# Kernel optimization log

Measured on AMD Instinct MI355X. Metric: run time of the kernel, lower is better.

Reference implementation:

```python
import math
import jax, jax.numpy as jnp
import numpy as np

B, S, HIDDEN = 1, 8192, 2048
NUM_HEADS = 16
HEAD_DIM = HIDDEN // NUM_HEADS
NUM_FW = 4
FW_DIM = HIDDEN // NUM_FW
D_H = FW_DIM  # inter_multi = 1.0
WINDOW = 256
CHUNK = 2048
ROPE_THETA = 500000.0
BASE_LR_INV = float(np.log(np.expm1(0.001)))  # inv_softplus(1e-3)


def rms_norm(x, w, eps=1e-6):
    return x * jax.lax.rsqrt(jnp.mean(x * x, axis=-1, keepdims=True) + eps) * w


def apply_rope(q, k, theta):
    D = q.shape[-1]
    inv = 1.0 / (theta ** (jnp.arange(0, D, 2, dtype=jnp.float32) / D))
    t = jnp.arange(q.shape[1], dtype=jnp.float32)
    f = t[:, None] * inv[None, :]  # [S, D/2]
    cos = jnp.cos(f)[None, :, None, :]
    sin = jnp.sin(f)[None, :, None, :]
    def ap(x):
        x1, x2 = jnp.split(x, 2, axis=-1)
        return jnp.concatenate([x1 * cos - x2 * sin, x2 * cos + x1 * sin], axis=-1)
    return ap(q), ap(k)


def sliding_window_attn(q, k, v, window):
    # q,k,v: [B,S,H,D]; causal window of `window` tokens incl. self (flash (window-1, 0))
    B_, S_, H_, D_ = q.shape
    W = window
    nc = S_ // W
    def blk(x):
        return x.transpose(0, 2, 1, 3).reshape(B_, H_, nc, W, D_)
    qb, kb, vb = blk(q), blk(k), blk(v)
    pad = jnp.zeros((B_, H_, 1, W, D_), q.dtype)
    k2 = jnp.concatenate([jnp.concatenate([pad, kb[:, :, :-1]], 2), kb], 3)  # [B,H,nc,2W,D]
    v2 = jnp.concatenate([jnp.concatenate([pad, vb[:, :, :-1]], 2), vb], 3)
    r = jnp.arange(W)[:, None]
    j = jnp.arange(2 * W)[None, :]
    base = (j >= r + 1) & (j <= W + r)  # causal + within-window
    keypos = (jnp.arange(nc)[:, None, None] - 1) * W + j[None]
    mask = base[None] & (keypos >= 0)  # [nc,W,2W]
    scores = jnp.einsum('bhnqd,bhnkd->bhnqk', qb, k2) * (1.0 / math.sqrt(D_))
    scores = jnp.where(mask[None, None], scores, -jnp.inf)
    p = jax.nn.softmax(scores, axis=-1)
    o = jnp.einsum('bhnqk,bhnkd->bhnqd', p, v2)
    return o.reshape(B_, H_, S_, D_).transpose(0, 2, 1, 3)


def ttt_swiglu(fq, fk, fv, l0, l1, l2, w0, w1, w2, chunk):
    # fq/fk/fv: [BN,S,d]; l*: [BN,S,1]; w0,w2: [BN,dh,d]; w1: [BN,d,dh]
    BN, S_, d = fq.shape
    nc = S_ // chunk
    def ch(x):
        return x.reshape(BN, nc, chunk, x.shape[-1]).transpose(1, 0, 2, 3)
    xs = (ch(fq), ch(fk), ch(fv), ch(l0), ch(l1), ch(l2))
    def step(carry, x):
        w0c, w1c, w2c = carry
        qi, ki, vi, lr0, lr1, lr2 = x
        # apply current fast weights to chunk queries (SwiGLU MLP)
        o = jnp.einsum('bch,boh->bco',
                       jax.nn.silu(jnp.einsum('bcd,bhd->bch', qi, w0c)) * jnp.einsum('bcd,bhd->bch', qi, w2c),
                       w1c)
        # manual gradient of dot-product TTT loss L = -sum(v * f(k))
        g = jnp.einsum('bcd,bhd->bch', ki, w0c)
        hm = jnp.einsum('bcd,bhd->bch', ki, w2c)
        sg = jax.nn.sigmoid(g)
        silu_g = g * sg
        hid = silu_g * hm
        dhid = jnp.einsum('bco,boh->bch', vi, w1c)
        dhm = dhid * silu_g
        dg = dhid * hm
        dgp = dg * (sg * (1.0 + g * (1.0 - sg)))  # silu backprop
        w0n = w0c + jnp.einsum('bch,bcd->bhd', dgp * lr0, ki)
        w2n = w2c + jnp.einsum('bch,bcd->bhd', dhm * lr2, ki)
        w1n = w1c + jnp.einsum('bco,bch->boh', vi * lr1, hid)
        return (w0n, w1n, w2n), o
    _, outs = jax.lax.scan(step, (w0, w1, w2), xs)
    return outs.transpose(1, 0, 2, 3).reshape(BN, S_, d)


def setup_inputs():
    key = jax.random.key(0)
    ks = jax.random.split(key, 8)
    h = HIDDEN
    return {
        'hidden_states': jax.random.normal(ks[0], (B, S, h), jnp.float32),
        'qkv_w': jax.random.normal(ks[1], (3 * h, h), jnp.float32) * 0.02,
        'q_norm_w': jnp.ones((h,), jnp.float32),
        'k_norm_w': jnp.ones((h,), jnp.float32),
        'qk_scale': jnp.ones((h, 2), jnp.float32),
        'qk_offset': jnp.zeros((h, 2), jnp.float32),
        'lr_w': jax.random.normal(ks[2], (3 * NUM_FW, h), jnp.float32) * 0.02,
        'lr_b': jnp.zeros((3 * NUM_FW,), jnp.float32),
        'w0': jax.random.normal(ks[3], (NUM_FW, D_H, FW_DIM), jnp.float32) / math.sqrt(FW_DIM),
        'w1': jax.random.normal(ks[4], (NUM_FW, FW_DIM, D_H), jnp.float32) / math.sqrt(D_H),
        'w2': jax.random.normal(ks[5], (NUM_FW, D_H, FW_DIM), jnp.float32) / math.sqrt(FW_DIM),
        'ttt_norm_w': jnp.ones((FW_DIM,), jnp.float32),
        'o_proj_w': jax.random.normal(ks[6], (h, h), jnp.float32) * 0.02,
    }


def reference(hidden_states, qkv_w, q_norm_w, k_norm_w, qk_scale, qk_offset,
              lr_w, lr_b, w0, w1, w2, ttt_norm_w, o_proj_w):
    qkv = hidden_states @ qkv_w.T
    q, k, v = jnp.split(qkv, 3, axis=-1)
    q = rms_norm(q, q_norm_w)
    k = rms_norm(k, k_norm_w)
    # rescale q/k for the fast-weight path
    fq = q * qk_scale[:, 0] + qk_offset[:, 0]
    fk = k * qk_scale[:, 1] + qk_offset[:, 1]
    fv = v
    # windowed RoPE attention path
    qh = q.reshape(B, S, NUM_HEADS, HEAD_DIM)
    kh = k.reshape(B, S, NUM_HEADS, HEAD_DIM)
    vh = v.reshape(B, S, NUM_HEADS, HEAD_DIM)
    qh, kh = apply_rope(qh, kh, ROPE_THETA)
    attn_o = sliding_window_attn(qh, kh, vh, WINDOW).reshape(B, S, HIDDEN)
    # fast-weight (TTT) path: silu + per-head l2-norm on q/k
    fq = jax.nn.silu(fq).reshape(B, S, NUM_FW, FW_DIM)
    fk = jax.nn.silu(fk).reshape(B, S, NUM_FW, FW_DIM)
    fv = jax.nn.silu(fv).reshape(B, S, NUM_FW, FW_DIM)
    fq = fq / jnp.maximum(jnp.linalg.norm(fq, axis=-1, keepdims=True), 1e-12)
    fk = fk / jnp.maximum(jnp.linalg.norm(fk, axis=-1, keepdims=True), 1e-12)
    def flat(x):
        return x.transpose(0, 2, 1, 3).reshape(B * NUM_FW, S, FW_DIM)
    # per-token learning rates (mamba parameterization)
    lr = jax.nn.softplus(hidden_states @ lr_w.T + lr_b + BASE_LR_INV)  # [B,S,3*NH]
    l0, l1, l2 = jnp.split(lr, 3, axis=-1)
    def flat_lr(x):
        return x.transpose(0, 2, 1).reshape(B * NUM_FW, S, 1)
    def bcast(w):
        return jnp.broadcast_to(w[None], (B,) + w.shape).reshape(B * NUM_FW, w.shape[1], w.shape[2])
    o_fast = ttt_swiglu(flat(fq), flat(fk), flat(fv),
                        flat_lr(l0), flat_lr(l1), flat_lr(l2),
                        bcast(w0), bcast(w1), bcast(w2), CHUNK)
    o_fast = rms_norm(o_fast.reshape(B, NUM_FW, S, FW_DIM), ttt_norm_w)
    o_fast = o_fast.transpose(0, 2, 1, 3).reshape(B, S, HIDDEN)
    return (attn_o + o_fast) @ o_proj_w.T
```

## Files before the change

### kernel.cpp

```cpp
#include <hip/hip_runtime.h>
#include <hip/hip_bf16.h>

typedef __hip_bfloat16 bf16;
typedef __bf16 bft;
typedef bft bf16x8 __attribute__((ext_vector_type(8)));
typedef bft bf16x4 __attribute__((ext_vector_type(4)));
typedef float f32x4 __attribute__((ext_vector_type(4)));

#define S_LEN 8192
#define HID   2048
#define QKV3  6144
#define NH    16
#define HD    128
#define NFW   4
#define FD    512
#define CHUNK_LEN 2048
#define NCHUNK 4
#define BASE_LR_INV (-6.9072552f)
#define QKP 136
#define VSP 72
#define PSP 76

__device__ __forceinline__ float bf2f(bf16 x){ return __bfloat162float(x); }
__device__ __forceinline__ bf16  f2bf(float x){ return __float2bfloat16(x); }
__device__ __forceinline__ float sigm(float x){ return 1.f/(1.f+__expf(-x)); }
__device__ __forceinline__ float siluf(float x){ return x/(1.f+__expf(-x)); }
__device__ __forceinline__ float wave_sum(float v){
  #pragma unroll
  for(int off=32; off; off>>=1) v += __shfl_xor(v, off, 64);
  return v;
}

template<int N>
__device__ __forceinline__ void waitcnt_vm(){
  static_assert(N==0||N==2||N==4||N==8, "unsupported vmcnt");
  if constexpr (N==0)      asm volatile("s_waitcnt vmcnt(0)" ::: "memory");
  else if constexpr (N==2) asm volatile("s_waitcnt vmcnt(2)" ::: "memory");
  else if constexpr (N==4) asm volatile("s_waitcnt vmcnt(4)" ::: "memory");
  else                     asm volatile("s_waitcnt vmcnt(8)" ::: "memory");
}

template<int ROWS>
__device__ __forceinline__ void stage(const bft* __restrict__ src, long ld,
                                      bft* dst, int tid)
{
  const int lane = tid & 63, wv = tid >> 6;
  #pragma unroll
  for (int i = 0; i < ROWS/64; ++i) {
    const int r0 = wv*16 + i*64;
    const int row = r0 + (lane >> 2);
    const int g = (lane & 3) ^ ((row >> 1) & 3);
    const bft* gp = src + (size_t)row*ld + g*8;
    bft* lp = dst + (size_t)r0*32;
    __builtin_amdgcn_global_load_lds(
        (const __attribute__((address_space(1))) void*)gp,
        (__attribute__((address_space(3))) void*)lp, 16, 0, 0);
  }
}

template<int BM,int BN,int EPI>
__global__ __launch_bounds__(256) void mgemm_k(
    const bft* __restrict__ A, const bft* __restrict__ B, void* __restrict__ Cv,
    bft* __restrict__ Cd, bft* __restrict__ Ct, int K,
    long lda, long ldb, long ldc, long sA, long sB, long sC)
{
  constexpr int AM = BM/32, AN = BN/32;
  constexpr int LPS = BM/64 + BN/64;
  __shared__ __align__(16) bft As[4][BM*32];
  __shared__ __align__(16) bft Bs[4][BN*32];
  const int tid = threadIdx.x;
  const int z = blockIdx.z;
  A += (size_t)z * sA;
  B += (size_t)z * sB;
  const size_t m0 = (size_t)blockIdx.y * BM, n0 = (size_t)blockIdx.x * BN;
  const int wv = tid >> 6, lane = tid & 63;
  const int wm = (wv & 1) * (BM/2), wn = (wv >> 1) * (BN/2);
  const int fr = lane & 15;
  const int fsw = ((lane >> 4) ^ ((fr >> 1) & 3)) * 8;

  f32x4 acc[AM][AN];
  #pragma unroll
  for (int i=0;i<AM;i++)
    #pragma unroll
    for (int j=0;j<AN;j++) acc[i][j] = (f32x4){0.f,0.f,0.f,0.f};

  const bft* Ab = A + m0*lda;
  const bft* Bb = B + n0*ldb;
  const int NS = K >> 5;

  stage<BM>(Ab,      lda, As[0], tid);
  stage<BN>(Bb,      ldb, Bs[0], tid);
  stage<BM>(Ab + 32, lda, As[1], tid);
  stage<BN>(Bb + 32, ldb, Bs[1], tid);

  auto compute = [&](int s){
    const bft* Ap = As[s & 3];
    const bft* Bp = Bs[s & 3];
    bf16x8 af[AM], bfv[AN];
    #pragma unroll
    for (int mi=0; mi<AM; mi++)
      af[mi] = *(const bf16x8*)(Ap + (size_t)(wm + mi*16 + fr)*32 + fsw);
    #pragma unroll
    for (int ni=0; ni<AN; ni++)
      bfv[ni] = *(const bf16x8*)(Bp + (size_t)(wn + ni*16 + fr)*32 + fsw);
    __builtin_amdgcn_s_setprio(1);
    #pragma unroll
    for (int mi=0; mi<AM; mi++)
      #pragma unroll
      for (int ni=0; ni<AN; ni++)
        acc[mi][ni] = __builtin_amdgcn_mfma_f32_16x16x32_bf16(af[mi], bfv[ni], acc[mi][ni], 0, 0, 0);
    __builtin_amdgcn_s_setprio(0);
  };

  for (int s = 0; s < NS - 2; ++s) {
    const int kt = (s + 2) * 32;
    stage<BM>(Ab + kt, lda, As[(s+2)&3], tid);
    stage<BN>(Bb + kt, ldb, Bs[(s+2)&3], tid);
    waitcnt_vm<2*LPS>();
    __builtin_amdgcn_s_barrier();
    asm volatile("" ::: "memory");
    compute(s);
  }
  waitcnt_vm<LPS>();
  __builtin_amdgcn_s_barrier();
  asm volatile("" ::: "memory");
  compute(NS - 2);
  waitcnt_vm<0>();
  __builtin_amdgcn_s_barrier();
  asm volatile("" ::: "memory");
  compute(NS - 1);

  const int er = (lane >> 4) * 4;
  const int ec = lane & 15;
  #pragma unroll
  for (int mi=0; mi<AM; mi++){
    #pragma unroll
    for (int ni=0; ni<AN; ni++){
      #pragma unroll
      for (int r=0; r<4; r++){
        size_t row = m0 + wm + mi*16 + er + r;
        size_t col = n0 + wn + ni*16 + ec;
        size_t idx = (size_t)z*sC + row*ldc + col;
        float v = acc[mi][ni][r];
        if constexpr (EPI == 0){
          ((bft*)Cv)[idx] = (bft)v;
        } else if constexpr (EPI == 1){
          ((float*)Cv)[idx] = v;
        } else {
          float nv = ((float*)Cv)[idx] + v;
          ((float*)Cv)[idx] = nv;
          Cd[idx] = (bft)nv;
          if (Ct) Ct[(size_t)z*FD*FD + col*FD + row] = (bft)nv;
        }
      }
    }
  }
}

template<int BM,int BN,int EPI>
static inline void mgemm(hipStream_t st, const bft* A, const bft* B, void* C,
    bft* Cd, bft* Ct, int M, int N, int K, long lda, long ldb, long ldc,
    int batch, long sA, long sB, long sC)
{
  dim3 g(N/BN, M/BM, batch);
  mgemm_k<BM,BN,EPI><<<g, 256, 0, st>>>(A, B, C, Cd, Ct, K, lda, ldb, ldc, sA, sB, sC);
}

__device__ __forceinline__ void stage8(const bft* __restrict__ src, long ld,
                                       bft* dst, int tid)
{
  const int lane = tid & 63, wv = tid >> 6;
  #pragma unroll
  for (int i = 0; i < 2; ++i) {
    const int r0 = wv*16 + i*128;
    const int row = r0 + (lane >> 2);
    const int g = (lane & 3) ^ ((row >> 1) & 3);
    const bft* gp = src + (size_t)row*ld + g*8;
    bft* lp = dst + (size_t)r0*32;
    __builtin_amdgcn_global_load_lds(
        (const __attribute__((address_space(1))) void*)gp,
        (__attribute__((address_space(3))) void*)lp, 16, 0, 0);
  }
}

template<int EPI>
__global__ __launch_bounds__(512, 2) void mgemm8_k(
    const bft* __restrict__ A, const bft* __restrict__ B, void* __restrict__ Cv,
    int K, long lda, long ldb, long ldc)
{
  __shared__ __align__(16) bft As[4][256*32];
  __shared__ __align__(16) bft Bs[4][256*32];
  const int tid = threadIdx.x;

  const int gx = (int)gridDim.x;
  const int nwg = (int)(gridDim.x * gridDim.y);
  int lin = (int)(blockIdx.y * gridDim.x + blockIdx.x);
  if ((nwg & 7) == 0) lin = (lin & 7) * (nwg >> 3) + (lin >> 3);
  const size_t m0 = (size_t)(lin / gx) * 256;
  const size_t n0 = (size_t)(lin % gx) * 256;

  const int wv = tid >> 6, lane = tid & 63;
  const int wm = (wv & 1) * 128, wn = (wv >> 1) * 64;
  const int fr = lane & 15;
  const int fsw = ((lane >> 4) ^ ((fr >> 1) & 3)) * 8;

  f32x4 acc[8][4];
  #pragma unroll
  for (int i=0;i<8;i++)
    #pragma unroll
    for (int j=0;j<4;j++) acc[i][j] = (f32x4){0.f,0.f,0.f,0.f};

  const bft* Ab = A + m0*lda;
  const bft* Bb = B + n0*ldb;
  const int NS = K >> 5;

  stage8(Ab,      lda, As[0], tid);
  stage8(Bb,      ldb, Bs[0], tid);
  stage8(Ab + 32, lda, As[1], tid);
  stage8(Bb + 32, ldb, Bs[1], tid);

  auto compute = [&](int s){
    const bft* Ap = As[s & 3];
    const bft* Bp = Bs[s & 3];
    bf16x8 af[8], bv[4];
    #pragma unroll
    for (int mi=0; mi<8; mi++)
      af[mi] = *(const bf16x8*)(Ap + (size_t)(wm + mi*16 + fr)*32 + fsw);
    #pragma unroll
    for (int ni=0; ni<4; ni++)
      bv[ni] = *(const bf16x8*)(Bp + (size_t)(wn + ni*16 + fr)*32 + fsw);
    __builtin_amdgcn_s_setprio(1);
    #pragma unroll
    for (int mi=0; mi<8; mi++)
      #pragma unroll
      for (int ni=0; ni<4; ni++)
        acc[mi][ni] = __builtin_amdgcn_mfma_f32_16x16x32_bf16(af[mi], bv[ni], acc[mi][ni], 0, 0, 0);
    __builtin_amdgcn_s_setprio(0);
  };

  for (int s = 0; s < NS - 2; ++s) {
    const int kt = (s + 2) * 32;
    stage8(Ab + kt, lda, As[(s+2)&3], tid);
    stage8(Bb + kt, ldb, Bs[(s+2)&3], tid);
    asm volatile("s_waitcnt vmcnt(8)" ::: "memory");
    __builtin_amdgcn_s_barrier();
    asm volatile("" ::: "memory");
    compute(s);
  }
  asm volatile("s_waitcnt vmcnt(4)" ::: "memory");
  __builtin_amdgcn_s_barrier();
  asm volatile("" ::: "memory");
  compute(NS - 2);
  asm volatile("s_waitcnt vmcnt(0)" ::: "memory");
  __builtin_amdgcn_s_barrier();
  asm volatile("" ::: "memory");
  compute(NS - 1);

  const int er = (lane >> 4) * 4;
  const int ec = lane & 15;
  #pragma unroll
  for (int mi=0; mi<8; mi++){
    #pragma unroll
    for (int ni=0; ni<4; ni++){
      #pragma unroll
      for (int r=0; r<4; r++){
        size_t row = m0 + wm + mi*16 + er + r;
        size_t col = n0 + wn + ni*16 + ec;
        size_t idx = row*ldc + col;
        float v = acc[mi][ni][r];
        if constexpr (EPI == 0) ((bft*)Cv)[idx] = (bft)v;
        else                    ((float*)Cv)[idx] = v;
      }
    }
  }
}

template<int EPI>
static inline void mgemm8(hipStream_t st, const bft* A, const bft* B, void* C,
                          int M, int N, int K, long lda, long ldb, long ldc)
{
  dim3 g(N/256, M/256, 1);
  mgemm8_k<EPI><<<g, 512, 0, st>>>(A, B, C, K, lda, ldb, ldc);
}

__global__ __launch_bounds__(256) void cvt_k(const float* __restrict__ s,
    bft* __restrict__ d)
{
  size_t i = ((size_t)blockIdx.x*256 + threadIdx.x) * 8;
  const float4 v0 = *(const float4*)(s + i);
  const float4 v1 = *(const float4*)(s + i + 4);
  bf16x8 b;
  b[0]=(bft)v0.x; b[1]=(bft)v0.y; b[2]=(bft)v0.z; b[3]=(bft)v0.w;
  b[4]=(bft)v1.x; b[5]=(bft)v1.y; b[6]=(bft)v1.z; b[7]=(bft)v1.w;
  *(bf16x8*)(d + i) = b;
}

__global__ __launch_bounds__(256) void tr_k(const bft* __restrict__ in,
    bft* __restrict__ out, long ldin, long sIn, long sOut)
{
  __shared__ __align__(16) bft t[64][72];
  const int c0 = blockIdx.x*64, r0 = blockIdx.y*64;
  in  += (size_t)blockIdx.z * sIn;
  out += (size_t)blockIdx.z * sOut;
  const int tid = threadIdx.x;
  #pragma unroll
  for (int i=0;i<2;i++){
    int e = tid + i*256;
    int r = e >> 3, c8 = (e & 7) * 8;
    *(bf16x8*)&t[r][c8] = *(const bf16x8*)(in + (size_t)(r0+r)*ldin + c0 + c8);
  }
  __syncthreads();
  #pragma unroll
  for (int i=0;i<2;i++){
    int e = tid + i*256;
    int c = e >> 3, r8 = (e & 7) * 8;
    bf16x8 v;
    #pragma unroll
    for (int j=0;j<8;j++) v[j] = t[r8+j][c];
    *(bf16x8*)(out + (size_t)(c0+c)*CHUNK_LEN + r0 + r8) = v;
  }
}

__global__ __launch_bounds__(256) void tcw1_k(const float* __restrict__ w1,
    bft* __restrict__ w1tb)
{
  size_t idx = (size_t)blockIdx.x*256 + threadIdx.x;
  int z = (int)(idx >> 18);
  int h = (int)((idx >> 9) & 511);
  int o = (int)(idx & 511);
  w1tb[idx] = (bft)w1[(size_t)z*FD*FD + (size_t)o*FD + h];
}

__global__ __launch_bounds__(256) void vt_k(const bf16* __restrict__ qkv,
    bft* __restrict__ vT)
{
  __shared__ __align__(16) bft t[64*QKP];
  const int s0 = blockIdx.x * 64;
  const int h  = blockIdx.y;
  const int tid = threadIdx.x;
  #pragma unroll
  for (int i=0;i<4;i++){
    int e = tid + i*256;
    int rr = e >> 4, doff = (e & 15) * 8;
    *(bf16x8*)(t + rr*QKP + doff) =
        *(const bf16x8*)((const bft*)qkv + (size_t)(s0+rr)*QKV3 + 2*HID + h*HD + doff);
  }
  __syncthreads();
  #pragma unroll
  for (int it=0; it<4; it++){
    int d = (tid >> 3) + it*32;
    int so8 = (tid & 7) * 8;
    bf16x8 v;
    #pragma unroll
    for (int j=0;j<8;j++) v[j] = t[(so8+j)*QKP + d];
    *(bf16x8*)(vT + ((size_t)(h*HD + d))*S_LEN + s0 + so8) = v;
  }
}

__global__ void rope_k(float* __restrict__ rc, float* __restrict__ rs){
  int pos = blockIdx.x, d = threadIdx.x;
  float inv = 1.f / powf(500000.0f, (float)d * (1.0f/64.0f));
  float ang = (float)pos * inv;
  rc[pos*64+d] = cosf(ang);
  rs[pos*64+d] = sinf(ang);
}

__global__ __launch_bounds__(256) void lr_k(const float* __restrict__ hidden,
    const float* __restrict__ lr_w, const float* __restrict__ lr_b,
    float* __restrict__ lro)
{
  __shared__ float hrow[HID];
  __shared__ float red[4][12];
  int s = blockIdx.x, tid = threadIdx.x;
  for(int i=0;i<HID/256;i++) hrow[tid+256*i] = hidden[(size_t)s*HID + tid + 256*i];
  __syncthreads();
  float part[12];
  #pragma unroll
  for(int o=0;o<12;o++) part[o]=0.f;
  for(int i=0;i<HID/256;i++){
    int j = tid + 256*i;
    float h = hrow[j];
    #pragma unroll
    for(int o=0;o<12;o++) part[o] += h * lr_w[o*HID + j];
  }
  int lane = tid & 63, w = tid >> 6;
  #pragma unroll
  for(int o=0;o<12;o++){
    float v = wave_sum(part[o]);
    if(lane==0) red[w][o] = v;
  }
  __syncthreads();
  if(tid < 12){
    float v = red[0][tid]+red[1][tid]+red[2][tid]+red[3][tid] + lr_b[tid] + BASE_LR_INV;
    float sp = (v > 20.f) ? v : log1pf(expf(v));
    lro[s*12 + tid] = sp;
  }
}

__global__ __launch_bounds__(256) void e2a_k(
    bf16* __restrict__ qkv,
    const float* __restrict__ qnw, const float* __restrict__ knw)
{
  __shared__ float red[8];
  int s = blockIdx.x, tid = threadIdx.x;
  int lane = tid & 63, w = tid >> 6;
  float qv[8], kv[8];
  float sq = 0.f, sk = 0.f;
  size_t base = (size_t)s*QKV3;
  #pragma unroll
  for(int i=0;i<8;i++){
    int j = tid*8 + i;
    qv[i] = bf2f(qkv[base + j]);
    kv[i] = bf2f(qkv[base + HID + j]);
    sq += qv[i]*qv[i]; sk += kv[i]*kv[i];
  }
  sq = wave_sum(sq); sk = wave_sum(sk);
  if(lane==0){ red[w] = sq; red[4+w] = sk; }
  __syncthreads();
  float rq = rsqrtf((red[0]+red[1]+red[2]+red[3])*(1.f/HID) + 1e-6f);
  float rk = rsqrtf((red[4]+red[5]+red[6]+red[7])*(1.f/HID) + 1e-6f);
  #pragma unroll
  for(int i=0;i<8;i++){
    int j = tid*8 + i;
    qkv[base + j]       = f2bf(qv[i]*rq*qnw[j]);
    qkv[base + HID + j] = f2bf(kv[i]*rk*knw[j]);
  }
}

__global__ __launch_bounds__(256) void e2b_k(
    bf16* __restrict__ qkv,
    const float* __restrict__ qks, const float* __restrict__ qko)
{
  int s = blockIdx.x, tid = threadIdx.x;
  size_t base = (size_t)s*QKV3;
  float a[8], b[8], vv[8];
  float ga = 0.f, gb2 = 0.f;
  #pragma unroll
  for(int i=0;i<8;i++){
    int j = tid*8 + i;
    float qn = bf2f(qkv[base + j]);
    float kn = bf2f(qkv[base + HID + j]);
    float v  = bf2f(qkv[base + 2*HID + j]);
    a[i] = siluf(qn*qks[2*j]   + qko[2*j]);
    b[i] = siluf(kn*qks[2*j+1] + qko[2*j+1]);
    vv[i] = siluf(v);
    ga += a[i]*a[i]; gb2 += b[i]*b[i];
  }
  ga = wave_sum(ga); gb2 = wave_sum(gb2);
  float iq = 1.f / fmaxf(sqrtf(ga), 1e-12f);
  float ik = 1.f / fmaxf(sqrtf(gb2), 1e-12f);
  #pragma unroll
  for(int i=0;i<8;i++){
    int j = tid*8 + i;
    qkv[base + j]         = f2bf(a[i]*iq);
    qkv[base + HID + j]   = f2bf(b[i]*ik);
    qkv[base + 2*HID + j] = f2bf(vv[i]);
  }
}

__global__ __launch_bounds__(256) void attn_k(
    const bf16* __restrict__ qkv, const bft* __restrict__ vT,
    const float* __restrict__ rc, const float* __restrict__ rs,
    float* __restrict__ attn)
{
  __shared__ __align__(16) bft Qs[64*QKP];
  __shared__ __align__(16) bft Ks[64*QKP];
  __shared__ __align__(16) bft Vs[128*VSP];
  __shared__ __align__(16) bft Ps[64*PSP];
  const int head = blockIdx.x >> 7;
  const int Q0 = (blockIdx.x & 127) * 64;
  const int tid = threadIdx.x;
  const int hb = head * HD;
  const int lane = tid & 63;
  const int wm = (tid >> 6) * 16;
  const int fr = lane & 15, fko = (lane >> 4) * 8;
  const int rbase = (lane >> 4) * 4;

  #pragma unroll
  for(int i=0;i<16;i++){
    int e = tid + i*256;
    int rr = e >> 6, d = e & 63;
    int qpos = Q0 + rr;
    size_t b = (size_t)qpos*QKV3 + hb;
    float x1 = bf2f(qkv[b + d]);
    float x2 = bf2f(qkv[b + d + 64]);
    float c = rc[qpos*64 + d], sn = rs[qpos*64 + d];
    Qs[rr*QKP + d]      = (bft)(x1*c - x2*sn);
    Qs[rr*QKP + d + 64] = (bft)(x2*c + x1*sn);
  }
  __syncthreads();
  bf16x8 qf[4];
  #pragma unroll
  for (int kk=0;kk<4;kk++)
    qf[kk] = *(const bf16x8*)(Qs + (wm+fr)*QKP + kk*32 + fko);

  f32x4 Ot[8];
  #pragma unroll
  for (int i=0;i<8;i++) Ot[i] = (f32x4){0.f,0.f,0.f,0.f};
  float m4[4], l4[4];
  #pragma unroll
  for (int r=0;r<4;r++){ m4[r] = -INFINITY; l4[r] = 0.f; }

  for (int kt=0; kt<5; kt++){
    const int kb = Q0 - 256 + kt*64;
    if (kb < 0) continue;
    __syncthreads();
    #pragma unroll
    for(int i=0;i<16;i++){
      int e = tid + i*256;
      int rr = e >> 6, d = e & 63;
      int kpos = kb + rr;
      size_t b = (size_t)kpos*QKV3 + HID + hb;
      float x1 = bf2f(qkv[b + d]);
      float x2 = bf2f(qkv[b + d + 64]);
      float c = rc[kpos*64 + d], sn = rs[kpos*64 + d];
      Ks[rr*QKP + d]      = (bft)(x1*c - x2*sn);
      Ks[rr*QKP + d + 64] = (bft)(x2*c + x1*sn);
    }
    {
      int d = tid >> 1, koff = (tid & 1) * 32;
      const bft* vrow = vT + ((size_t)(hb + d))*S_LEN + kb + koff;
      bft* lrow = Vs + d*VSP + koff;
      #pragma unroll
      for (int j8=0;j8<4;j8++)
        *(bf16x8*)(lrow + j8*8) = *(const bf16x8*)(vrow + j8*8);
    }
    __syncthreads();

    f32x4 st[4];
    #pragma unroll
    for (int nt=0;nt<4;nt++){
      f32x4 acc = (f32x4){0.f,0.f,0.f,0.f};
      #pragma unroll
      for (int kk=0;kk<4;kk++){
        bf16x8 kf = *(const bf16x8*)(Ks + (nt*16+fr)*QKP + kk*32 + fko);
        acc = __builtin_amdgcn_mfma_f32_16x16x32_bf16(qf[kk], kf, acc, 0, 0, 0);
      }
      st[nt] = acc;
    }

    float pv[4][4];
    #pragma unroll
    for (int r=0;r<4;r++){
      int qpos = Q0 + wm + rbase + r;
      float sm[4];
      float mx = -INFINITY;
      #pragma unroll
      for (int nt=0;nt<4;nt++){
        int kpos = kb + nt*16 + fr;
        bool valid = (kpos > qpos - 256) && (kpos <= qpos);
        float s = valid ? st[nt][r] * 0.088388347648318447f : -INFINITY;
        sm[nt] = s;
        mx = fmaxf(mx, s);
      }
      mx = fmaxf(mx, __shfl_xor(mx, 1, 64));
      mx = fmaxf(mx, __shfl_xor(mx, 2, 64));
      mx = fmaxf(mx, __shfl_xor(mx, 4, 64));
      mx = fmaxf(mx, __shfl_xor(mx, 8, 64));
      float mnew = fmaxf(m4[r], mx);
      float alpha = (mnew == -INFINITY) ? 1.f : __expf(m4[r] - mnew);
      float ps = 0.f;
      #pragma unroll
      for (int nt=0;nt<4;nt++){
        float p = (sm[nt] == -INFINITY) ? 0.f : __expf(sm[nt] - mnew);
        pv[nt][r] = p;
        ps += p;
      }
      ps += __shfl_xor(ps, 1, 64);
      ps += __shfl_xor(ps, 2, 64);
      ps += __shfl_xor(ps, 4, 64);
      ps += __shfl_xor(ps, 8, 64);
      l4[r] = l4[r]*alpha + ps;
      m4[r] = mnew;
      #pragma unroll
      for (int ct=0;ct<8;ct++) Ot[ct][r] *= alpha;
    }

    #pragma unroll
    for (int r=0;r<4;r++){
      int row = wm + rbase + r;
      #pragma unroll
      for (int nt=0;nt<4;nt++)
        Ps[row*PSP + nt*16 + fr] = (bft)pv[nt][r];
    }
    bf16x8 af[2];
    #pragma unroll
    for (int kk=0;kk<2;kk++){
      const bft* pp = Ps + (wm+fr)*PSP + kk*32 + fko;
      bf16x4 lo = *(const bf16x4*)pp;
      bf16x4 hi = *(const bf16x4*)(pp+4);
      bf16x8 a;
      #pragma unroll
      for (int j=0;j<4;j++){ a[j]=lo[j]; a[j+4]=hi[j]; }
      af[kk]=a;
    }
    #pragma unroll
    for (int ct=0;ct<8;ct++)
      #pragma unroll
      for (int kk=0;kk<2;kk++){
        bf16x8 bv = *(const bf16x8*)(Vs + (ct*16+fr)*VSP + kk*32 + fko);
        Ot[ct] = __builtin_amdgcn_mfma_f32_16x16x32_bf16(af[kk], bv, Ot[ct], 0, 0, 0);
      }
  }

  #pragma unroll
  for (int r=0;r<4;r++){
    float invl = 1.f / l4[r];
    int qpos = Q0 + wm + rbase + r;
    size_t ob = (size_t)qpos*HID + hb;
    #pragma unroll
    for (int ct=0;ct<8;ct++)
      attn[ob + ct*16 + fr] = Ot[ct][r] * invl;
  }
}

__global__ __launch_bounds__(256) void e3_k(
    const bf16* __restrict__ g, const bf16* __restrict__ hm,
    bf16* __restrict__ qg, const bf16* __restrict__ qm,
    bf16* __restrict__ hid)
{
  size_t idx = (size_t)blockIdx.x*256 + threadIdx.x;
  float opre = siluf(bf2f(qg[idx])) * bf2f(qm[idx]);
  hid[idx] = f2bf(siluf(bf2f(g[idx])) * bf2f(hm[idx]));
  qg[idx]  = f2bf(opre);
}

__global__ __launch_bounds__(256) void e4_k(
    bf16* __restrict__ g, bf16* __restrict__ hm, bf16* __restrict__ dhid,
    const bf16* __restrict__ qkv, const float* __restrict__ lrb, int cbase)
{
  size_t idx = (size_t)blockIdx.x*256 + threadIdx.x;
  int h  = (int)(idx >> 20);
  int ci = (int)((idx >> 9) & 2047);
  int d  = (int)(idx & 511);
  int s  = cbase + ci;
  float l0  = lrb[s*12 + h];
  float l1  = lrb[s*12 + 4 + h];
  float l2v = lrb[s*12 + 8 + h];
  float gg = bf2f(g[idx]), hv = bf2f(hm[idx]), dh = bf2f(dhid[idx]);
  float sg = sigm(gg);
  float silu_g = gg * sg;
  float dhm = dh * silu_g;
  float dg  = dh * hv;
  float dgp = dg * (sg * (1.f + gg * (1.f - sg)));
  float fvv = bf2f(qkv[(size_t)s*QKV3 + 2*HID + h*FD + d]);
  g[idx]    = f2bf(dgp * l0);
  hm[idx]   = f2bf(dhm * l2v);
  dhid[idx] = f2bf(fvv * l1);
}

__global__ __launch_bounds__(256) void e5_k(const float* __restrict__ attn,
    const bf16* __restrict__ ofc, const float* __restrict__ tnw,
    bf16* __restrict__ qkv, int cbase)
{
  int ci = blockIdx.x, tid = threadIdx.x;
  int s = cbase + ci;
  int lane = tid & 63, w = tid >> 6;
  float o[8]; float ss = 0.f;
  size_t ob = ((size_t)w*CHUNK_LEN + ci)*FD + (size_t)lane*8;
  #pragma unroll
  for(int i=0;i<8;i++){ o[i] = bf2f(ofc[ob+i]); ss += o[i]*o[i]; }
  ss = wave_sum(ss);
  float inv = rsqrtf(ss*(1.f/FD) + 1e-6f);
  size_t xb = (size_t)s*QKV3 + w*FD + (size_t)lane*8;
  size_t ab = (size_t)s*HID  + w*FD + (size_t)lane*8;
  #pragma unroll
  for(int i=0;i<8;i++){
    int d = lane*8 + i;
    qkv[xb+i] = f2bf(attn[ab+i] + o[i]*inv*tnw[d]);
  }
}

extern "C" void kernel_launch(void* const* d_in, const int* in_sizes, int n_in,
                              void* d_out, int out_size, void* d_ws, size_t ws_size,
                              hipStream_t stream)
{
  (void)in_sizes; (void)n_in; (void)out_size;
  const float* hidden   = (const float*)d_in[0];
  const float* qkv_w    = (const float*)d_in[1];
  const float* q_norm_w = (const float*)d_in[2];
  const float* k_norm_w = (const float*)d_in[3];
  const float* qk_scale = (const float*)d_in[4];
  const float* qk_off   = (const float*)d_in[5];
  const float* lr_w     = (const float*)d_in[6];
  const float* lr_b     = (const float*)d_in[7];
  const float* w0_in    = (const float*)d_in[8];
  const float* w1_in    = (const float*)d_in[9];
  const float* w2_in    = (const float*)d_in[10];
  const float* ttt_nw   = (const float*)d_in[11];
  const float* o_proj   = (const float*)d_in[12];
  float* out = (float*)d_out;

  char* p = (char*)d_ws;
  auto alloc = [&](size_t n){ char* r = p; p += (n + 255) & ~(size_t)255; return (void*)r; };

  bf16*  qkv   = (bf16*) alloc((size_t)S_LEN*QKV3*sizeof(bf16));
  float* lrb   = (float*)alloc((size_t)S_LEN*12*sizeof(float));
  float* rc    = (float*)alloc((size_t)S_LEN*64*sizeof(float));
  float* rs    = (float*)alloc((size_t)S_LEN*64*sizeof(float));
  float* w0s   = (float*)alloc((size_t)NFW*FD*FD*sizeof(float));
  float* w1s   = (float*)alloc((size_t)NFW*FD*FD*sizeof(float));
  float* w2s   = (float*)alloc((size_t)NFW*FD*FD*sizeof(float));
  bft*   w1tb  = (bft*)  alloc((size_t)NFW*FD*FD*sizeof(bft));
  bft*   w0b   = (bft*)  alloc((size_t)NFW*FD*FD*sizeof(bft));
  bft*   w1b   = (bft*)  alloc((size_t)NFW*FD*FD*sizeof(bft));
  bft*   w2b   = (bft*)  alloc((size_t)NFW*FD*FD*sizeof(bft));
  bf16*  gb    = (bf16*) alloc((size_t)NFW*CHUNK_LEN*FD*sizeof(bf16));
  bf16*  hmb   = (bf16*) alloc((size_t)NFW*CHUNK_LEN*FD*sizeof(bf16));
  bf16*  qgb   = (bf16*) alloc((size_t)NFW*CHUNK_LEN*FD*sizeof(bf16));
  bf16*  qmb   = (bf16*) alloc((size_t)NFW*CHUNK_LEN*FD*sizeof(bf16));
  bf16*  hidb  = (bf16*) alloc((size_t)NFW*CHUNK_LEN*FD*sizeof(bf16));
  bf16*  ofc   = (bf16*) alloc((size_t)NFW*CHUNK_LEN*FD*sizeof(bf16));
  bft*   fkT   = (bft*)  alloc((size_t)NFW*FD*CHUNK_LEN*sizeof(bft));
  bft*   hidT  = (bft*)  alloc((size_t)NFW*FD*CHUNK_LEN*sizeof(bft));
  bft*   a2T   = (bft*)  alloc((size_t)NFW*FD*CHUNK_LEN*sizeof(bft));
  bft*   a1T   = (bft*)  alloc((size_t)NFW*FD*CHUNK_LEN*sizeof(bft));

  if ((size_t)(p - (char*)d_ws) > ws_size) return;

  bft* hidden_bf = (bft*)gb;
  bft* qkvw_bf   = (bft*)fkT;
  bft* vT        = (bft*)fkT;
  bft* opw_bf    = (bft*)hidb;

  float* attn = out;

  hipMemcpyAsync(w0s, w0_in, (size_t)NFW*FD*FD*sizeof(float), hipMemcpyDeviceToDevice, stream);
  hipMemcpyAsync(w1s, w1_in, (size_t)NFW*FD*FD*sizeof(float), hipMemcpyDeviceToDevice, stream);
  hipMemcpyAsync(w2s, w2_in, (size_t)NFW*FD*FD*sizeof(float), hipMemcpyDeviceToDevice, stream);

  rope_k<<<S_LEN, 64, 0, stream>>>(rc, rs);
  lr_k<<<S_LEN, 256, 0, stream>>>(hidden, lr_w, lr_b, lrb);
  tcw1_k<<<NFW*FD*FD/256, 256, 0, stream>>>(w1_in, w1tb);
  cvt_k<<<(NFW*FD*FD)/2048, 256, 0, stream>>>(w0_in, w0b);
  cvt_k<<<(NFW*FD*FD)/2048, 256, 0, stream>>>(w1_in, w1b);
  cvt_k<<<(NFW*FD*FD)/2048, 256, 0, stream>>>(w2_in, w2b);
  cvt_k<<<(S_LEN*HID)/2048, 256, 0, stream>>>(hidden, hidden_bf);
  cvt_k<<<(QKV3*HID)/2048, 256, 0, stream>>>(qkv_w, qkvw_bf);

  mgemm8<0>(stream, hidden_bf, qkvw_bf, (void*)qkv, S_LEN, QKV3, HID, HID, HID, QKV3);

  e2a_k<<<S_LEN, 256, 0, stream>>>(qkv, q_norm_w, k_norm_w);
  vt_k<<<dim3(S_LEN/64, NH), 256, 0, stream>>>(qkv, vT);
  attn_k<<<NH*128, 256, 0, stream>>>(qkv, vT, rc, rs, attn);
  e2b_k<<<S_LEN, 256, 0, stream>>>(qkv, qk_scale, qk_off);

  const long sW  = (long)FD*FD;
  const long sCh = (long)CHUNK_LEN*FD;
  const long sT  = (long)FD*CHUNK_LEN;
  const int  NEL = NFW*CHUNK_LEN*FD/256;
  const dim3 tg(FD/64, CHUNK_LEN/64, NFW);

  for(int c=0; c<NCHUNK; c++){
    const bft* fqc = (const bft*)qkv + (size_t)c*CHUNK_LEN*QKV3;
    const bft* fkc = fqc + HID;
    const bft* fvc = fqc + 2*HID;
    mgemm<128,128,0>(stream, fkc, w0b, gb,  nullptr, nullptr, CHUNK_LEN, FD, FD, QKV3, FD, FD, NFW, FD, sW, sCh);
    mgemm<128,128,0>(stream, fkc, w2b, hmb, nullptr, nullptr, CHUNK_LEN, FD, FD, QKV3, FD, FD, NFW, FD, sW, sCh);
    mgemm<128,128,0>(stream, fqc, w0b, qgb, nullptr, nullptr, CHUNK_LEN, FD, FD, QKV3, FD, FD, NFW, FD, sW, sCh);
    mgemm<128,128,0>(stream, fqc, w2b, qmb, nullptr, nullptr, CHUNK_LEN, FD, FD, QKV3, FD, FD, NFW, FD, sW, sCh);
    e3_k<<<NEL, 256, 0, stream>>>(gb, hmb, qgb, qmb, hidb);
    mgemm<128,128,0>(stream, (const bft*)qgb, w1b, ofc, nullptr, nullptr, CHUNK_LEN, FD, FD, FD, FD, FD, NFW, sCh, sW, sCh);
    mgemm<128,128,0>(stream, fvc, (const bft*)w1tb, qmb, nullptr, nullptr, CHUNK_LEN, FD, FD, QKV3, FD, FD, NFW, FD, sW, sCh);
    e4_k<<<NEL, 256, 0, stream>>>(gb, hmb, qmb, qkv, lrb, c*CHUNK_LEN);
    tr_k<<<tg, 256, 0, stream>>>(fkc,              fkT,        QKV3, FD,  sT);
    tr_k<<<tg, 256, 0, stream>>>((const bft*)hidb, hidT,       FD,   sCh, sT);
    tr_k<<<tg, 256, 0, stream>>>((const bft*)gb,   (bft*)qgb,  FD,   sCh, sT);
    tr_k<<<tg, 256, 0, stream>>>((const bft*)hmb,  a2T,        FD,   sCh, sT);
    tr_k<<<tg, 256, 0, stream>>>((const bft*)qmb,  a1T,        FD,   sCh, sT);
    mgemm<64,64,2>(stream, (const bft*)qgb, fkT,  w0s, w0b, nullptr, FD, FD, CHUNK_LEN, CHUNK_LEN, CHUNK_LEN, FD, NFW, sT, sT, sW);
    mgemm<64,64,2>(stream, a2T,             fkT,  w2s, w2b, nullptr, FD, FD, CHUNK_LEN, CHUNK_LEN, CHUNK_LEN, FD, NFW, sT, sT, sW);
    mgemm<64,64,2>(stream, a1T,             hidT, w1s, w1b, w1tb,    FD, FD, CHUNK_LEN, CHUNK_LEN, CHUNK_LEN, FD, NFW, sT, sT, sW);
    e5_k<<<CHUNK_LEN, 256, 0, stream>>>(attn, ofc, ttt_nw, qkv, c*CHUNK_LEN);
  }

  cvt_k<<<(HID*HID)/2048, 256, 0, stream>>>(o_proj, opw_bf);
  mgemm8<1>(stream, (const bft*)qkv, opw_bf, out, S_LEN, HID, HID, QKV3, HID, HID);
}
```

Before: 1.578 ms.

## Split GEMM K-step into barrier-separated phases interleaving LDS reads, staging and MFMA

Both MFMA GEMM kernels are restructured so each K-step is split into phases. Each phase loads part of the A fragments from LDS, issues part of the next global-to-LDS stage, then runs a batch of MFMAs, with workgroup barriers and scheduling barriers between phases. The goal is to overlap LDS reads, global loads and matrix math across waves and to cut register pressure by holding fewer A fragments at once. The cost is more barriers per K-step and a more delicate vmcnt/buffer-reuse protocol, which risks stalls or races if the wait counts are off.

```diff
diff --git a/kernel.cpp b/kernel.cpp
--- a/kernel.cpp
+++ b/kernel.cpp
@@ -40,6 +40,13 @@
   else                     asm volatile("s_waitcnt vmcnt(8)" ::: "memory");
 }
 
+__device__ __forceinline__ void phase_edge(){
+  __builtin_amdgcn_sched_barrier(0);
+  __builtin_amdgcn_s_barrier();
+  asm volatile("" ::: "memory");
+  __builtin_amdgcn_sched_barrier(0);
+}
+
 template<int ROWS>
 __device__ __forceinline__ void stage(const bft* __restrict__ src, long ld,
                                       bft* dst, int tid)
@@ -65,7 +72,9 @@
     long lda, long ldb, long ldc, long sA, long sB, long sC)
 {
   constexpr int AM = BM/32, AN = BN/32;
-  constexpr int LPS = BM/64 + BN/64;
+  constexpr int LPT = BM/64 + BN/64;
+  constexpr int NPH = (AM >= 4) ? 2 : 1;
+  constexpr int MH  = AM / NPH;
   __shared__ __align__(16) bft As[4][BM*32];
   __shared__ __align__(16) bft Bs[4][BN*32];
   const int tid = threadIdx.x;
@@ -92,43 +101,53 @@
   stage<BN>(Bb,      ldb, Bs[0], tid);
   stage<BM>(Ab + 32, lda, As[1], tid);
   stage<BN>(Bb + 32, ldb, Bs[1], tid);
-
-  auto compute = [&](int s){
+  waitcnt_vm<LPT>();
+  __builtin_amdgcn_s_barrier();
+  asm volatile("" ::: "memory");
+
+  for (int s = 0; s < NS; ++s) {
     const bft* Ap = As[s & 3];
     const bft* Bp = Bs[s & 3];
-    bf16x8 af[AM], bfv[AN];
-    #pragma unroll
-    for (int mi=0; mi<AM; mi++)
-      af[mi] = *(const bf16x8*)(Ap + (size_t)(wm + mi*16 + fr)*32 + fsw);
+    const int kt = (s + 2) * 32;
+    const bool st = (s + 2 < NS);
+
+    bf16x8 bvv[AN], afv[MH];
     #pragma unroll
     for (int ni=0; ni<AN; ni++)
-      bfv[ni] = *(const bf16x8*)(Bp + (size_t)(wn + ni*16 + fr)*32 + fsw);
+      bvv[ni] = *(const bf16x8*)(Bp + (size_t)(wn + ni*16 + fr)*32 + fsw);
+    #pragma unroll
+    for (int i=0; i<MH; i++)
+      afv[i] = *(const bf16x8*)(Ap + (size_t)(wm + i*16 + fr)*32 + fsw);
+    if (st) stage<BM>(Ab + kt, lda, As[(s+2)&3], tid);
+    if constexpr (NPH == 1) {
+      if (st) { stage<BN>(Bb + kt, ldb, Bs[(s+2)&3], tid); waitcnt_vm<LPT>(); }
+      else waitcnt_vm<0>();
+    }
+    phase_edge();
     __builtin_amdgcn_s_setprio(1);
     #pragma unroll
-    for (int mi=0; mi<AM; mi++)
+    for (int i=0; i<MH; i++)
       #pragma unroll
       for (int ni=0; ni<AN; ni++)
-        acc[mi][ni] = __builtin_amdgcn_mfma_f32_16x16x32_bf16(af[mi], bfv[ni], acc[mi][ni], 0, 0, 0);
+        acc[i][ni] = __builtin_amdgcn_mfma_f32_16x16x32_bf16(afv[i], bvv[ni], acc[i][ni], 0, 0, 0);
     __builtin_amdgcn_s_setprio(0);
-  };
-
-  for (int s = 0; s < NS - 2; ++s) {
-    const int kt = (s + 2) * 32;
-    stage<BM>(Ab + kt, lda, As[(s+2)&3], tid);
-    stage<BN>(Bb + kt, ldb, Bs[(s+2)&3], tid);
-    waitcnt_vm<2*LPS>();
-    __builtin_amdgcn_s_barrier();
-    asm volatile("" ::: "memory");
-    compute(s);
-  }
-  waitcnt_vm<LPS>();
-  __builtin_amdgcn_s_barrier();
-  asm volatile("" ::: "memory");
-  compute(NS - 2);
-  waitcnt_vm<0>();
-  __builtin_amdgcn_s_barrier();
-  asm volatile("" ::: "memory");
-  compute(NS - 1);
+
+    if constexpr (NPH == 2) {
+      #pragma unroll
+      for (int i=0; i<MH; i++)
+        afv[i] = *(const bf16x8*)(Ap + (size_t)(wm + (MH+i)*16 + fr)*32 + fsw);
+      if (st) { stage<BN>(Bb + kt, ldb, Bs[(s+2)&3], tid); waitcnt_vm<LPT>(); }
+      else waitcnt_vm<0>();
+      phase_edge();
+      __builtin_amdgcn_s_setprio(1);
+      #pragma unroll
+      for (int i=0; i<MH; i++)
+        #pragma unroll
+        for (int ni=0; ni<AN; ni++)
+          acc[MH+i][ni] = __builtin_amdgcn_mfma_f32_16x16x32_bf16(afv[i], bvv[ni], acc[MH+i][ni], 0, 0, 0);
+      __builtin_amdgcn_s_setprio(0);
+    }
+  }
 
   const int er = (lane >> 4) * 4;
   const int ec = lane & 15;
@@ -183,6 +202,12 @@
   }
 }
 
+#define M8_ROW(mi, a) { \
+    acc[mi][0]=__builtin_amdgcn_mfma_f32_16x16x32_bf16(a,bv[0],acc[mi][0],0,0,0); \
+    acc[mi][1]=__builtin_amdgcn_mfma_f32_16x16x32_bf16(a,bv[1],acc[mi][1],0,0,0); \
+    acc[mi][2]=__builtin_amdgcn_mfma_f32_16x16x32_bf16(a,bv[2],acc[mi][2],0,0,0); \
+    acc[mi][3]=__builtin_amdgcn_mfma_f32_16x16x32_bf16(a,bv[3],acc[mi][3],0,0,0); }
+
 template<int EPI>
 __global__ __launch_bounds__(512, 2) void mgemm8_k(
     const bft* __restrict__ A, const bft* __restrict__ B, void* __restrict__ Cv,
@@ -218,43 +243,52 @@
   stage8(Bb,      ldb, Bs[0], tid);
   stage8(Ab + 32, lda, As[1], tid);
   stage8(Bb + 32, ldb, Bs[1], tid);
-
-  auto compute = [&](int s){
+  waitcnt_vm<4>();
+  __builtin_amdgcn_s_barrier();
+  asm volatile("" ::: "memory");
+
+  for (int s = 0; s < NS; ++s) {
     const bft* Ap = As[s & 3];
     const bft* Bp = Bs[s & 3];
-    bf16x8 af[8], bv[4];
-    #pragma unroll
-    for (int mi=0; mi<8; mi++)
-      af[mi] = *(const bf16x8*)(Ap + (size_t)(wm + mi*16 + fr)*32 + fsw);
-    #pragma unroll
-    for (int ni=0; ni<4; ni++)
-      bv[ni] = *(const bf16x8*)(Bp + (size_t)(wn + ni*16 + fr)*32 + fsw);
+    const int kt = (s + 2) * 32;
+    const bool st = (s + 2 < NS);
+    bf16x8 bv[4], a0, a1;
+
+    bv[0] = *(const bf16x8*)(Bp + (size_t)(wn +  0 + fr)*32 + fsw);
+    bv[1] = *(const bf16x8*)(Bp + (size_t)(wn + 16 + fr)*32 + fsw);
+    bv[2] = *(const bf16x8*)(Bp + (size_t)(wn + 32 + fr)*32 + fsw);
+    bv[3] = *(const bf16x8*)(Bp + (size_t)(wn + 48 + fr)*32 + fsw);
+    a0 = *(const bf16x8*)(Ap + (size_t)(wm +  0 + fr)*32 + fsw);
+    a1 = *(const bf16x8*)(Ap + (size_t)(wm + 16 + fr)*32 + fsw);
+    if (st) stage8(Ab + kt, lda, As[(s+2)&3], tid);
+    phase_edge();
     __builtin_amdgcn_s_setprio(1);
-    #pragma unroll
-    for (int mi=0; mi<8; mi++)
-      #pragma unroll
-      for (int ni=0; ni<4; ni++)
-        acc[mi][ni] = __builtin_amdgcn_mfma_f32_16x16x32_bf16(af[mi], bv[ni], acc[mi][ni], 0, 0, 0);
+    M8_ROW(0, a0); M8_ROW(1, a1);
     __builtin_amdgcn_s_setprio(0);
-  };
-
-  for (int s = 0; s < NS - 2; ++s) {
-    const int kt = (s + 2) * 32;
-    stage8(Ab + kt, lda, As[(s+2)&3], tid);
-    stage8(Bb + kt, ldb, Bs[(s+2)&3], tid);
-    asm volatile("s_waitcnt vmcnt(8)" ::: "memory");
-    __builtin_amdgcn_s_barrier();
-    asm volatile("" ::: "memory");
-    compute(s);
-  }
-  asm volatile("s_waitcnt vmcnt(4)" ::: "memory");
-  __builtin_amdgcn_s_barrier();
-  asm volatile("" ::: "memory");
-  compute(NS - 2);
-  asm volatile("s_waitcnt vmcnt(0)" ::: "memory");
-  __builtin_amdgcn_s_barrier();
-  asm volatile("" ::: "memory");
-  compute(NS - 1);
+
+    a0 = *(const bf16x8*)(Ap + (size_t)(wm + 32 + fr)*32 + fsw);
+    a1 = *(const bf16x8*)(Ap + (size_t)(wm + 48 + fr)*32 + fsw);
+    if (st) stage8(Bb + kt, ldb, Bs[(s+2)&3], tid);
+    phase_edge();
+    __builtin_amdgcn_s_setprio(1);
+    M8_ROW(2, a0); M8_ROW(3, a1);
+    __builtin_amdgcn_s_setprio(0);
+
+    a0 = *(const bf16x8*)(Ap + (size_t)(wm + 64 + fr)*32 + fsw);
+    a1 = *(const bf16x8*)(Ap + (size_t)(wm + 80 + fr)*32 + fsw);
+    phase_edge();
+    __builtin_amdgcn_s_setprio(1);
+    M8_ROW(4, a0); M8_ROW(5, a1);
+    __builtin_amdgcn_s_setprio(0);
+
+    a0 = *(const bf16x8*)(Ap + (size_t)(wm +  96 + fr)*32 + fsw);
+    a1 = *(const bf16x8*)(Ap + (size_t)(wm + 112 + fr)*32 + fsw);
+    if (st) waitcnt_vm<4>(); else waitcnt_vm<0>();
+    phase_edge();
+    __builtin_amdgcn_s_setprio(1);
+    M8_ROW(6, a0); M8_ROW(7, a1);
+    __builtin_amdgcn_s_setprio(0);
+  }
 
   const int er = (lane >> 4) * 4;
   const int ec = lane & 15;
```

New measurement: 1.563 ms. Within noise of the previous version (-0.9%).
